# Performance work log

Measured on AMD Instinct MI355X. Metric: run time of the kernel, lower is better.

The kernel has to match this reference:

```python
import jax, jax.numpy as jnp
import numpy as np

N_HEAD = 12

def setup_inputs() -> dict:
    key = jax.random.key(0)
    k1, k2, k3, k4, k5 = jax.random.split(key, 5)
    B, T, C = 16, 1024, 768
    s = 0.02
    return {
        "x": jax.random.normal(k1, (B, T, C), dtype=jnp.float32),
        "W_attn": jax.random.normal(k2, (C, 3 * C), dtype=jnp.float32) * s,
        "b_attn": jax.random.normal(k3, (3 * C,), dtype=jnp.float32) * s,
        "W_proj": jax.random.normal(k4, (C, C), dtype=jnp.float32) * s,
        "b_proj": jax.random.normal(k5, (C,), dtype=jnp.float32) * s,
    }

def reference(x, W_attn, b_attn, W_proj, b_proj):
    B, T, C = x.shape
    H = N_HEAD
    d = C // H
    qkv = x @ W_attn + b_attn                      # [B,T,3C]
    q, k, v = jnp.split(qkv, 3, axis=-1)
    # [B,H,T,d]
    q = q.reshape(B, T, H, d).transpose(0, 2, 1, 3)
    k = k.reshape(B, T, H, d).transpose(0, 2, 1, 3)
    v = v.reshape(B, T, H, d).transpose(0, 2, 1, 3)
    scale = 1.0 / jnp.sqrt(jnp.array(d, dtype=x.dtype))
    att = jnp.einsum('bhqd,bhkd->bhqk', q, k) * scale   # [B,H,T,T]
    causal = jnp.tril(jnp.ones((T, T), dtype=bool))
    att = jnp.where(causal[None, None], att, -jnp.inf)
    att = jax.nn.softmax(att, axis=-1)
    # dropout is identity in eval mode (p=0 for deterministic reference)
    y = jnp.einsum('bhqk,bhkd->bhqd', att, v)            # [B,H,T,d]
    y = y.transpose(0, 2, 1, 3).reshape(B, T, C)
    return y @ W_proj + b_proj
```

## Files before the change

kernel.cpp:

```cpp
#include <hip/hip_runtime.h>
#include <cstddef>


typedef __bf16 bf16_t;
typedef __bf16 bf16x4 __attribute__((ext_vector_type(4)));
typedef __bf16 bf16x8 __attribute__((ext_vector_type(8)));
typedef float  f32x4  __attribute__((ext_vector_type(4)));

#define MFMA16(a,b,c) __builtin_amdgcn_mfma_f32_16x16x32_bf16((a),(b),(c),0,0,0)
#define GLOAD16(gp, lp) \
  __builtin_amdgcn_global_load_lds((const __attribute__((address_space(1))) unsigned int*)(gp), \
                                   (__attribute__((address_space(3))) unsigned int*)(lp), 16, 0, 0)

#define SWZ(row, c) (((row) * 64) + ((((c) ^ ((row) & 7)) * 8)))

#define QSCALE 0.1803368801111f

__global__ __launch_bounds__(256)
void prep_kernel(const float* __restrict__ x, bf16_t* __restrict__ Xb,
                 const float* __restrict__ Wa, bf16_t* __restrict__ WaT,
                 const float* __restrict__ Wp, bf16_t* __restrict__ WpT)
{
    __shared__ bf16_t tile[32][33];
    const int bx = blockIdx.x;
    if (bx < 12288) {
        const size_t i = ((size_t)bx * 256 + threadIdx.x) * 4;
        float4 f = *(const float4*)(x + i);
        bf16x4 o = {(bf16_t)f.x, (bf16_t)f.y, (bf16_t)f.z, (bf16_t)f.w};
        *(bf16x4*)(Xb + i) = o;
        return;
    }
    const float* in;  bf16_t* out;  int R, Cn, c0, r0;
    if (bx < 14016) {
        const int t = bx - 12288;
        in = Wa; out = WaT; R = 768; Cn = 2304;
        c0 = (t % 72) * 32; r0 = (t / 72) * 32;
    } else {
        const int t = bx - 14016;
        in = Wp; out = WpT; R = 768; Cn = 768;
        c0 = (t % 24) * 32; r0 = (t / 24) * 32;
    }
    const int tx = threadIdx.x & 31, ty = threadIdx.x >> 5;
#pragma unroll
    for (int i = 0; i < 4; ++i)
        tile[ty + i*8][tx] = (bf16_t)in[(size_t)(r0 + ty + i*8) * Cn + c0 + tx];
    __syncthreads();
#pragma unroll
    for (int i = 0; i < 4; ++i)
        out[(size_t)(c0 + ty + i*8) * R + r0 + tx] = tile[tx][ty + i*8];
}

#define LGKM0() asm volatile("s_waitcnt lgkmcnt(0)" ::: "memory")
#define VMC(n)  asm volatile("s_waitcnt vmcnt(" #n ")" ::: "memory")
#define PBAR()  __builtin_amdgcn_s_barrier()
#define PRIO1() __builtin_amdgcn_s_setprio(1)
#define PRIO0() __builtin_amdgcn_s_setprio(0)

#define STAGE_HT(buf, kt, ht) do { \
    if ((ht) == 0) { \
        const int r0_ = w * 16; \
        GLOAD16(WT + (size_t)(nt + r0_ + lr) * 768 + (kt) + lcs,     &Bs[buf][r0_ * 64]); \
        GLOAD16(WT + (size_t)(nt + r0_ + 8 + lr) * 768 + (kt) + lcs, &Bs[buf][(r0_ + 8) * 64]); \
    } else if ((ht) == 1) { \
        const int r1_ = 128 + w * 8; \
        GLOAD16(WT + (size_t)(nt + r1_ + lr) * 768 + (kt) + lcs,     &Bs[buf][r1_ * 64]); \
    } else { \
        const int r0_ = w * 16 + (((ht) == 3) ? 128 : 0); \
        GLOAD16(Xb + (size_t)(mt + r0_ + lr) * 768 + (kt) + lcs,     &As[buf][r0_ * 64]); \
        GLOAD16(Xb + (size_t)(mt + r0_ + 8 + lr) * 768 + (kt) + lcs, &As[buf][(r0_ + 8) * 64]); \
    } \
} while (0)

#define RD_BX(dst, buf) do { \
    _Pragma("unroll") for (int j_ = 0; j_ < 4; ++j_) \
    _Pragma("unroll") for (int ks_ = 0; ks_ < 2; ++ks_) \
        (dst)[j_][ks_] = *(const bf16x8*)(&As[buf][SWZ(wc * 64 + j_ * 16 + lm, ks_ * 4 + lq)]); \
} while (0)

#define RD_AW(dst, buf, F0, NF) do { \
    _Pragma("unroll") for (int p_ = 0; p_ < (NF); ++p_) \
    _Pragma("unroll") for (int ks_ = 0; ks_ < 2; ++ks_) \
        (dst)[p_][ks_] = *(const bf16x8*)(&Bs[buf][SWZ(wr * 96 + ((F0) + p_) * 16 + lm, ks_ * 4 + lq)]); \
} while (0)

#define MFMA_G(AW, BX, F0, NP) do { \
    _Pragma("unroll") for (int ks_ = 0; ks_ < 2; ++ks_) \
    _Pragma("unroll") for (int p_ = 0; p_ < (NP); ++p_) \
    _Pragma("unroll") for (int j_ = 0; j_ < 4; ++j_) \
        acc[(F0) + p_][j_] = MFMA16((AW)[p_][ks_], (BX)[j_][ks_], acc[(F0) + p_][j_]); \
} while (0)

__global__ __launch_bounds__(512)
void qkv_gemm8(const bf16_t* __restrict__ Xb, const bf16_t* __restrict__ WT,
               const float* __restrict__ bias,
               bf16_t* __restrict__ Qb, bf16_t* __restrict__ Kb, bf16_t* __restrict__ VT)
{
    __shared__ bf16_t As[2][256 * 64];
    __shared__ bf16_t Bs[2][192 * 64];
    const int tid = threadIdx.x;
    const int w = tid >> 6, l = tid & 63;
    const int lm = l & 15, lq = l >> 4;
    const int lr = l >> 3;
    const int lcs = ((l & 7) ^ lr) * 8;
    const int wr = w >> 2, wc = w & 3;

    const int g = blockIdx.x;
    const int gt = (g & 7) * 96 + (g >> 3);
    const int bm = gt / 12, bn = gt % 12;
    const int mt = bm * 256, nt = bn * 192;

    f32x4 acc[6][4];
    const f32x4 z4 = {0.f, 0.f, 0.f, 0.f};
#pragma unroll
    for (int i = 0; i < 6; ++i)
#pragma unroll
        for (int j = 0; j < 4; ++j) acc[i][j] = z4;

    bf16x8 bx0[4][2], bx1[4][2];
    bf16x8 aw01[2][2], aw23[2][2], aw45[2][2];

    STAGE_HT(0, 0, 0); STAGE_HT(0, 0, 1); STAGE_HT(0, 0, 2); STAGE_HT(0, 0, 3);
    STAGE_HT(1, 64, 0); STAGE_HT(1, 64, 1);
    VMC(3);
    PBAR();
    RD_BX(bx0, 0); RD_AW(aw01, 0, 0, 2);

#pragma unroll 1
    for (int it = 0; it < 5; ++it) {
        const int kv = it * 128 + 64, ku2 = kv + 64, kv2 = ku2 + 64;
        RD_AW(aw23, 0, 2, 2);
        STAGE_HT(1, kv, 2);
        PBAR(); LGKM0();
        PRIO1(); MFMA_G(aw01, bx0, 0, 2); PRIO0();
        PBAR();
        RD_AW(aw45, 0, 4, 2);
        STAGE_HT(1, kv, 3);
        PBAR(); LGKM0();
        PRIO1(); MFMA_G(aw23, bx0, 2, 2); PRIO0();
        PBAR();
        STAGE_HT(0, ku2, 0);
        PBAR();
        PRIO1(); MFMA_G(&aw45[0], bx0, 4, 1); PRIO0();
        VMC(2);
        PBAR();
        RD_BX(bx1, 1); RD_AW(aw01, 1, 0, 2);
        STAGE_HT(0, ku2, 1);
        PBAR(); LGKM0();
        PRIO1(); MFMA_G(&aw45[1], bx0, 5, 1); PRIO0();
        PBAR();
        RD_AW(aw23, 1, 2, 2);
        STAGE_HT(0, ku2, 2);
        PBAR(); LGKM0();
        PRIO1(); MFMA_G(aw01, bx1, 0, 2); PRIO0();
        PBAR();
        RD_AW(aw45, 1, 4, 2);
        STAGE_HT(0, ku2, 3);
        PBAR(); LGKM0();
        PRIO1(); MFMA_G(aw23, bx1, 2, 2); PRIO0();
        PBAR();
        STAGE_HT(1, kv2, 0);
        PBAR();
        PRIO1(); MFMA_G(&aw45[0], bx1, 4, 1); PRIO0();
        VMC(2);
        PBAR();
        RD_BX(bx0, 0); RD_AW(aw01, 0, 0, 2);
        STAGE_HT(1, kv2, 1);
        PBAR(); LGKM0();
        PRIO1(); MFMA_G(&aw45[1], bx1, 5, 1); PRIO0();
        PBAR();
    }

    RD_AW(aw23, 0, 2, 2);
    STAGE_HT(1, 704, 2);
    PBAR(); LGKM0();
    PRIO1(); MFMA_G(aw01, bx0, 0, 2); PRIO0();
    PBAR();
    RD_AW(aw45, 0, 4, 2);
    STAGE_HT(1, 704, 3);
    PBAR(); LGKM0();
    PRIO1(); MFMA_G(aw23, bx0, 2, 2); PRIO0();
    PBAR();
    PRIO1(); MFMA_G(&aw45[0], bx0, 4, 1); MFMA_G(&aw45[1], bx0, 5, 1); PRIO0();
    VMC(0);
    PBAR();
    RD_BX(bx1, 1); RD_AW(aw01, 1, 0, 2);
    RD_AW(aw23, 1, 2, 2); RD_AW(aw45, 1, 4, 2);
    LGKM0();
    MFMA_G(aw01, bx1, 0, 2);
    MFMA_G(aw23, bx1, 2, 2);
    MFMA_G(&aw45[0], bx1, 4, 1);
    MFMA_G(&aw45[1], bx1, 5, 1);

    const int which = nt / 768;
    const int b_ = mt >> 10;
    const int tb = (mt & 1023) + wc * 64;
    if (which == 2) {
#pragma unroll
        for (int f = 0; f < 6; ++f) {
            const int nglob = nt + wr * 96 + f * 16 + lq * 4;
            const int nin = nglob - 1536;
            const int h = nin >> 6, d0 = nin & 63;
            bf16_t* vt = VT + (size_t)(b_ * 12 + h) * 65536;
            const float4 bv = *(const float4*)(bias + nglob);
#pragma unroll
            for (int j = 0; j < 4; ++j) {
                const int t = tb + j * 16 + lm;
                f32x4 v = acc[f][j];
                vt[(size_t)(d0 + 0) * 1024 + t] = (bf16_t)(v[0] + bv.x);
                vt[(size_t)(d0 + 1) * 1024 + t] = (bf16_t)(v[1] + bv.y);
                vt[(size_t)(d0 + 2) * 1024 + t] = (bf16_t)(v[2] + bv.z);
                vt[(size_t)(d0 + 3) * 1024 + t] = (bf16_t)(v[3] + bv.w);
            }
        }
    } else {
        bf16_t* dst = (which == 0) ? Qb : Kb;
        const float qs = (which == 0) ? QSCALE : 1.0f;
#pragma unroll
        for (int f = 0; f < 6; ++f) {
            const int nglob = nt + wr * 96 + f * 16 + lq * 4;
            const int nin = nglob - which * 768;
            const int h = nin >> 6, d0 = nin & 63;
            const float4 bv = *(const float4*)(bias + nglob);
#pragma unroll
            for (int j = 0; j < 4; ++j) {
                const int t = tb + j * 16 + lm;
                f32x4 v = acc[f][j];
                bf16x4 o4 = {(bf16_t)((v[0] + bv.x) * qs), (bf16_t)((v[1] + bv.y) * qs),
                             (bf16_t)((v[2] + bv.z) * qs), (bf16_t)((v[3] + bv.w) * qs)};
                *(bf16x4*)(dst + ((size_t)(b_ * 12 + h) * 1024 + t) * 64 + d0) = o4;
            }
        }
    }
}

__global__ __launch_bounds__(256, 3)
void attn_kernel(const bf16_t* __restrict__ Qb, const bf16_t* __restrict__ Kb,
                 const bf16_t* __restrict__ VT, bf16_t* __restrict__ Y)
{
    __shared__ bf16_t Ks[2][64 * 64];
    __shared__ bf16_t Vs[2][64 * 64];
    __shared__ bf16_t Plds[4 * 16 * 72];
    const int tid = threadIdx.x;
    const int w = tid >> 6, l = tid & 63;
    const int lm = l & 15, lq = l >> 4;
    const int lr = l >> 3;
    const int lc8 = ((l & 7) ^ lr) * 8;
    const int xp = blockIdx.x;
    const int bh = blockIdx.y;
    const int loq = xp * 128, hiq = (7 - xp) * 128;

    int qmin[4];
    qmin[0] = loq + w * 32;      qmin[1] = qmin[0] + 16;
    qmin[2] = hiq + w * 32;      qmin[3] = qmin[2] + 16;

    const bf16_t* Kbase = Kb + (size_t)bh * 65536;
    const bf16_t* Vbase = VT + (size_t)bh * 65536;
    bf16_t* Pw = &Plds[w * 1152];
    const int r0a = w * 16, r0b = w * 16 + 8;

    bf16x8 bq[4][2];
#pragma unroll
    for (int m = 0; m < 4; ++m) {
        const bf16_t* Qp = Qb + ((size_t)bh * 1024 + qmin[m] + lm) * 64;
        bq[m][0] = *(const bf16x8*)(Qp + lq * 8);
        bq[m][1] = *(const bf16x8*)(Qp + 32 + lq * 8);
    }

    f32x4 O[4][4];
    float li[4] = {0.f, 0.f, 0.f, 0.f};
    const f32x4 z4 = {0.f, 0.f, 0.f, 0.f};
#pragma unroll
    for (int m = 0; m < 4; ++m)
#pragma unroll
        for (int s = 0; s < 4; ++s) O[m][s] = z4;

    const int kend = hiq + 64;

    GLOAD16(Kbase + (size_t)(r0a + lr) * 64 + lc8,   &Ks[0][r0a * 64]);
    GLOAD16(Kbase + (size_t)(r0b + lr) * 64 + lc8,   &Ks[0][r0b * 64]);
    GLOAD16(Vbase + (size_t)(r0a + lr) * 1024 + lc8, &Vs[0][r0a * 64]);
    GLOAD16(Vbase + (size_t)(r0b + lr) * 1024 + lc8, &Vs[0][r0b * 64]);
    __syncthreads();

    int cb = 0;
    for (int k0 = 0; k0 <= kend; k0 += 64) {
        const int nxt = cb ^ 1;
        if (k0 + 64 <= kend) {
            const int kn = k0 + 64;
            if (nxt) {
                GLOAD16(Kbase + (size_t)(kn + r0a + lr) * 64 + lc8,        &Ks[1][r0a * 64]);
                GLOAD16(Kbase + (size_t)(kn + r0b + lr) * 64 + lc8,        &Ks[1][r0b * 64]);
                GLOAD16(Vbase + (size_t)(r0a + lr) * 1024 + kn + lc8,      &Vs[1][r0a * 64]);
                GLOAD16(Vbase + (size_t)(r0b + lr) * 1024 + kn + lc8,      &Vs[1][r0b * 64]);
            } else {
                GLOAD16(Kbase + (size_t)(kn + r0a + lr) * 64 + lc8,        &Ks[0][r0a * 64]);
                GLOAD16(Kbase + (size_t)(kn + r0b + lr) * 64 + lc8,        &Ks[0][r0b * 64]);
                GLOAD16(Vbase + (size_t)(r0a + lr) * 1024 + kn + lc8,      &Vs[0][r0a * 64]);
                GLOAD16(Vbase + (size_t)(r0b + lr) * 1024 + kn + lc8,      &Vs[0][r0b * 64]);
            }
        }
        const bf16_t* Kc = Ks[cb];
        const bf16_t* Vc = Vs[cb];
#pragma unroll
        for (int m = 0; m < 4; ++m) {
            if (k0 > qmin[m] + 15) continue;
            f32x4 S[4];
#pragma unroll
            for (int s = 0; s < 4; ++s) S[s] = z4;
#pragma unroll
            for (int ks = 0; ks < 2; ++ks)
#pragma unroll
                for (int s = 0; s < 4; ++s) {
                    bf16x8 ak = *(const bf16x8*)(&Kc[SWZ(s * 16 + lm, ks * 4 + lq)]);
                    S[s] = MFMA16(ak, bq[m][ks], S[s]);
                }
            if (k0 + 63 > qmin[m]) {
                const int q = qmin[m] + lm;
#pragma unroll
                for (int s = 0; s < 4; ++s)
#pragma unroll
                    for (int rg = 0; rg < 4; ++rg)
                        if (k0 + s * 16 + lq * 4 + rg > q) S[s][rg] = -1e30f;
            }
            float ls = 0.f;
#pragma unroll
            for (int s = 0; s < 4; ++s)
#pragma unroll
                for (int rg = 0; rg < 4; ++rg) {
                    float pv = exp2f(S[s][rg]);
                    S[s][rg] = pv;
                    ls += pv;
                }
            li[m] += ls;
#pragma unroll
            for (int s = 0; s < 4; ++s) {
                bf16x4 p4 = {(bf16_t)S[s][0], (bf16_t)S[s][1],
                             (bf16_t)S[s][2], (bf16_t)S[s][3]};
                *(bf16x4*)(&Pw[lm * 72 + s * 16 + lq * 4]) = p4;
            }
#pragma unroll
            for (int ks = 0; ks < 2; ++ks) {
                bf16x8 bp = *(const bf16x8*)(&Pw[lm * 72 + ks * 32 + lq * 8]);
#pragma unroll
                for (int s = 0; s < 4; ++s) {
                    bf16x8 av = *(const bf16x8*)(&Vc[SWZ(s * 16 + lm, ks * 4 + lq)]);
                    O[m][s] = MFMA16(av, bp, O[m][s]);
                }
            }
        }
        __syncthreads();
        cb = nxt;
    }

    const int b = bh / 12, h = bh % 12;
#pragma unroll
    for (int m = 0; m < 4; ++m) {
        float s0 = li[m];
        s0 += __shfl_xor(s0, 16, 64);
        s0 += __shfl_xor(s0, 32, 64);
        const float inv = 1.f / s0;
        const size_t row = ((size_t)(b * 1024 + qmin[m] + lm)) * 768 + h * 64;
#pragma unroll
        for (int s = 0; s < 4; ++s) {
            bf16x4 y4 = {(bf16_t)(O[m][s][0] * inv), (bf16_t)(O[m][s][1] * inv),
                         (bf16_t)(O[m][s][2] * inv), (bf16_t)(O[m][s][3] * inv)};
            *(bf16x4*)(Y + row + s * 16 + lq * 4) = y4;
        }
    }
}

__global__ __launch_bounds__(256)
void proj_gemm(const bf16_t* __restrict__ A, const bf16_t* __restrict__ WT,
               const float* __restrict__ bias, float* __restrict__ out)
{
    __shared__ bf16_t As[128 * 64];
    __shared__ bf16_t Bs[128 * 64];
    const int tid = threadIdx.x;
    const int w = tid >> 6, l = tid & 63;
    const int lm = l & 15, lq = l >> 4;
    const int wy = w >> 1, wx = w & 1;
    const int lr = l >> 3;
    const int lcs = ((l & 7) ^ lr) * 8;
    const int nt = blockIdx.x * 128, mt = blockIdx.y * 128;

    f32x4 acc[4][4];
    const f32x4 z4 = {0.f, 0.f, 0.f, 0.f};
#pragma unroll
    for (int i = 0; i < 4; ++i)
#pragma unroll
        for (int j = 0; j < 4; ++j) acc[i][j] = z4;

    for (int kt = 0; kt < 768; kt += 64) {
#pragma unroll
        for (int p = 0; p < 4; ++p) {
            const int row = w * 32 + p * 8;
            GLOAD16(A  + (size_t)(mt + row + lr) * 768 + kt + lcs, &As[row * 64]);
            GLOAD16(WT + (size_t)(nt + row + lr) * 768 + kt + lcs, &Bs[row * 64]);
        }
        __syncthreads();
#pragma unroll
        for (int ks = 0; ks < 2; ++ks) {
            const int c = ks * 4 + lq;
            bf16x8 aw[4], bx[4];
#pragma unroll
            for (int i = 0; i < 4; ++i)
                aw[i] = *(const bf16x8*)(&Bs[SWZ(wx * 64 + i * 16 + lm, c)]);
#pragma unroll
            for (int j = 0; j < 4; ++j)
                bx[j] = *(const bf16x8*)(&As[SWZ(wy * 64 + j * 16 + lm, c)]);
#pragma unroll
            for (int i = 0; i < 4; ++i)
#pragma unroll
                for (int j = 0; j < 4; ++j)
                    acc[i][j] = MFMA16(aw[i], bx[j], acc[i][j]);
        }
        __syncthreads();
    }
#pragma unroll
    for (int i = 0; i < 4; ++i) {
        const int n0 = nt + wx * 64 + i * 16 + lq * 4;
        const float4 bv = *(const float4*)(bias + n0);
#pragma unroll
        for (int j = 0; j < 4; ++j) {
            const int t = mt + wy * 64 + j * 16 + lm;
            f32x4 v = acc[i][j];
            float4 o = {v[0] + bv.x, v[1] + bv.y, v[2] + bv.z, v[3] + bv.w};
            *(float4*)(out + (size_t)t * 768 + n0) = o;
        }
    }
}

extern "C" void kernel_launch(void* const* d_in, const int* in_sizes, int n_in,
                              void* d_out, int out_size, void* d_ws, size_t ws_size,
                              hipStream_t stream)
{
    const float* x      = (const float*)d_in[0];
    const float* W_attn = (const float*)d_in[1];
    const float* b_attn = (const float*)d_in[2];
    const float* W_proj = (const float*)d_in[3];
    const float* b_proj = (const float*)d_in[4];
    float* out = (float*)d_out;

    char* ws = (char*)d_ws;
    const size_t SZ = (size_t)16 * 12 * 1024 * 64 * 2;
    bf16_t* Qb  = (bf16_t*)(ws);
    bf16_t* Kb  = (bf16_t*)(ws + SZ);
    bf16_t* VT  = (bf16_t*)(ws + 3 * SZ);
    bf16_t* Yb  = (bf16_t*)(ws + 4 * SZ);
    bf16_t* Xb  = (bf16_t*)(ws + 4 * SZ);
    bf16_t* WaT = (bf16_t*)(ws + 5 * SZ);
    bf16_t* WpT = (bf16_t*)(ws + 5 * SZ + (size_t)2304 * 768 * 2);

    prep_kernel<<<14592, 256, 0, stream>>>(x, Xb, W_attn, WaT, W_proj, WpT);
    qkv_gemm8<<<768, 512, 0, stream>>>(Xb, WaT, b_attn, Qb, Kb, VT);
    attn_kernel<<<dim3(4, 192), 256, 0, stream>>>(Qb, Kb, VT, Yb);
    proj_gemm<<<dim3(6, 128), 256, 0, stream>>>(Yb, WpT, b_proj, out);
}
```

Baseline: 275.3 us.

## Reuse pipelined 256x192 GEMM for projection, swizzle attention P buffer

Moves the software-pipelined double-buffered GEMM body of the QKV kernel into a shared macro and uses it for a new 256x192-tile output projection kernel with grouped block ordering. This replaces the simple single-buffered 128x128 proj_gemm. The attention kernel's padded P scratch in LDS becomes an XOR-swizzled unpadded layout, and its occupancy hint rises from 3 to 4 blocks per CU. The projection now launches only 256 blocks, which may underfill the GPU, and the higher attention occupancy target may force register spills.

```diff
diff --git a/kernel.cpp b/kernel.cpp
--- a/kernel.cpp
+++ b/kernel.cpp
@@ -90,6 +90,77 @@
         acc[(F0) + p_][j_] = MFMA16((AW)[p_][ks_], (BX)[j_][ks_], acc[(F0) + p_][j_]); \
 } while (0)
 
+#define GEMM8_BODY() \
+    STAGE_HT(0, 0, 0); STAGE_HT(0, 0, 1); STAGE_HT(0, 0, 2); STAGE_HT(0, 0, 3); \
+    STAGE_HT(1, 64, 0); STAGE_HT(1, 64, 1); \
+    VMC(3); \
+    PBAR(); \
+    RD_BX(bx0, 0); RD_AW(aw01, 0, 0, 2); \
+    _Pragma("unroll 1") \
+    for (int it = 0; it < 5; ++it) { \
+        const int kv = it * 128 + 64, ku2 = kv + 64, kv2 = ku2 + 64; \
+        RD_AW(aw23, 0, 2, 2); \
+        STAGE_HT(1, kv, 2); \
+        PBAR(); LGKM0(); \
+        PRIO1(); MFMA_G(aw01, bx0, 0, 2); PRIO0(); \
+        PBAR(); \
+        RD_AW(aw45, 0, 4, 2); \
+        STAGE_HT(1, kv, 3); \
+        PBAR(); LGKM0(); \
+        PRIO1(); MFMA_G(aw23, bx0, 2, 2); PRIO0(); \
+        PBAR(); \
+        STAGE_HT(0, ku2, 0); \
+        PBAR(); \
+        PRIO1(); MFMA_G(&aw45[0], bx0, 4, 1); PRIO0(); \
+        VMC(2); \
+        PBAR(); \
+        RD_BX(bx1, 1); RD_AW(aw01, 1, 0, 2); \
+        STAGE_HT(0, ku2, 1); \
+        PBAR(); LGKM0(); \
+        PRIO1(); MFMA_G(&aw45[1], bx0, 5, 1); PRIO0(); \
+        PBAR(); \
+        RD_AW(aw23, 1, 2, 2); \
+        STAGE_HT(0, ku2, 2); \
+        PBAR(); LGKM0(); \
+        PRIO1(); MFMA_G(aw01, bx1, 0, 2); PRIO0(); \
+        PBAR(); \
+        RD_AW(aw45, 1, 4, 2); \
+        STAGE_HT(0, ku2, 3); \
+        PBAR(); LGKM0(); \
+        PRIO1(); MFMA_G(aw23, bx1, 2, 2); PRIO0(); \
+        PBAR(); \
+        STAGE_HT(1, kv2, 0); \
+        PBAR(); \
+        PRIO1(); MFMA_G(&aw45[0], bx1, 4, 1); PRIO0(); \
+        VMC(2); \
+        PBAR(); \
+        RD_BX(bx0, 0); RD_AW(aw01, 0, 0, 2); \
+        STAGE_HT(1, kv2, 1); \
+        PBAR(); LGKM0(); \
+        PRIO1(); MFMA_G(&aw45[1], bx1, 5, 1); PRIO0(); \
+        PBAR(); \
+    } \
+    RD_AW(aw23, 0, 2, 2); \
+    STAGE_HT(1, 704, 2); \
+    PBAR(); LGKM0(); \
+    PRIO1(); MFMA_G(aw01, bx0, 0, 2); PRIO0(); \
+    PBAR(); \
+    RD_AW(aw45, 0, 4, 2); \
+    STAGE_HT(1, 704, 3); \
+    PBAR(); LGKM0(); \
+    PRIO1(); MFMA_G(aw23, bx0, 2, 2); PRIO0(); \
+    PBAR(); \
+    PRIO1(); MFMA_G(&aw45[0], bx0, 4, 1); MFMA_G(&aw45[1], bx0, 5, 1); PRIO0(); \
+    VMC(0); \
+    PBAR(); \
+    RD_BX(bx1, 1); RD_AW(aw01, 1, 0, 2); \
+    RD_AW(aw23, 1, 2, 2); RD_AW(aw45, 1, 4, 2); \
+    LGKM0(); \
+    MFMA_G(aw01, bx1, 0, 2); \
+    MFMA_G(aw23, bx1, 2, 2); \
+    MFMA_G(&aw45[0], bx1, 4, 1); \
+    MFMA_G(&aw45[1], bx1, 5, 1);
+
 __global__ __launch_bounds__(512)
 void qkv_gemm8(const bf16_t* __restrict__ Xb, const bf16_t* __restrict__ WT,
                const float* __restrict__ bias,
@@ -119,77 +190,7 @@
     bf16x8 bx0[4][2], bx1[4][2];
     bf16x8 aw01[2][2], aw23[2][2], aw45[2][2];
 
-    STAGE_HT(0, 0, 0); STAGE_HT(0, 0, 1); STAGE_HT(0, 0, 2); STAGE_HT(0, 0, 3);
-    STAGE_HT(1, 64, 0); STAGE_HT(1, 64, 1);
-    VMC(3);
-    PBAR();
-    RD_BX(bx0, 0); RD_AW(aw01, 0, 0, 2);
-
-#pragma unroll 1
-    for (int it = 0; it < 5; ++it) {
-        const int kv = it * 128 + 64, ku2 = kv + 64, kv2 = ku2 + 64;
-        RD_AW(aw23, 0, 2, 2);
-        STAGE_HT(1, kv, 2);
-        PBAR(); LGKM0();
-        PRIO1(); MFMA_G(aw01, bx0, 0, 2); PRIO0();
-        PBAR();
-        RD_AW(aw45, 0, 4, 2);
-        STAGE_HT(1, kv, 3);
-        PBAR(); LGKM0();
-        PRIO1(); MFMA_G(aw23, bx0, 2, 2); PRIO0();
-        PBAR();
-        STAGE_HT(0, ku2, 0);
-        PBAR();
-        PRIO1(); MFMA_G(&aw45[0], bx0, 4, 1); PRIO0();
-        VMC(2);
-        PBAR();
-        RD_BX(bx1, 1); RD_AW(aw01, 1, 0, 2);
-        STAGE_HT(0, ku2, 1);
-        PBAR(); LGKM0();
-        PRIO1(); MFMA_G(&aw45[1], bx0, 5, 1); PRIO0();
-        PBAR();
-        RD_AW(aw23, 1, 2, 2);
-        STAGE_HT(0, ku2, 2);
-        PBAR(); LGKM0();
-        PRIO1(); MFMA_G(aw01, bx1, 0, 2); PRIO0();
-        PBAR();
-        RD_AW(aw45, 1, 4, 2);
-        STAGE_HT(0, ku2, 3);
-        PBAR(); LGKM0();
-        PRIO1(); MFMA_G(aw23, bx1, 2, 2); PRIO0();
-        PBAR();
-        STAGE_HT(1, kv2, 0);
-        PBAR();
-        PRIO1(); MFMA_G(&aw45[0], bx1, 4, 1); PRIO0();
-        VMC(2);
-        PBAR();
-        RD_BX(bx0, 0); RD_AW(aw01, 0, 0, 2);
-        STAGE_HT(1, kv2, 1);
-        PBAR(); LGKM0();
-        PRIO1(); MFMA_G(&aw45[1], bx1, 5, 1); PRIO0();
-        PBAR();
-    }
-
-    RD_AW(aw23, 0, 2, 2);
-    STAGE_HT(1, 704, 2);
-    PBAR(); LGKM0();
-    PRIO1(); MFMA_G(aw01, bx0, 0, 2); PRIO0();
-    PBAR();
-    RD_AW(aw45, 0, 4, 2);
-    STAGE_HT(1, 704, 3);
-    PBAR(); LGKM0();
-    PRIO1(); MFMA_G(aw23, bx0, 2, 2); PRIO0();
-    PBAR();
-    PRIO1(); MFMA_G(&aw45[0], bx0, 4, 1); MFMA_G(&aw45[1], bx0, 5, 1); PRIO0();
-    VMC(0);
-    PBAR();
-    RD_BX(bx1, 1); RD_AW(aw01, 1, 0, 2);
-    RD_AW(aw23, 1, 2, 2); RD_AW(aw45, 1, 4, 2);
-    LGKM0();
-    MFMA_G(aw01, bx1, 0, 2);
-    MFMA_G(aw23, bx1, 2, 2);
-    MFMA_G(&aw45[0], bx1, 4, 1);
-    MFMA_G(&aw45[1], bx1, 5, 1);
+    GEMM8_BODY();
 
     const int which = nt / 768;
     const int b_ = mt >> 10;
@@ -233,13 +234,58 @@
     }
 }
 
-__global__ __launch_bounds__(256, 3)
+__global__ __launch_bounds__(512)
+void proj_gemm8(const bf16_t* __restrict__ Xb, const bf16_t* __restrict__ WT,
+                const float* __restrict__ bias, float* __restrict__ out)
+{
+    __shared__ bf16_t As[2][256 * 64];
+    __shared__ bf16_t Bs[2][192 * 64];
+    const int tid = threadIdx.x;
+    const int w = tid >> 6, l = tid & 63;
+    const int lm = l & 15, lq = l >> 4;
+    const int lr = l >> 3;
+    const int lcs = ((l & 7) ^ lr) * 8;
+    const int wr = w >> 2, wc = w & 3;
+
+    const int g = blockIdx.x;
+    const int gt = (g & 7) * 32 + (g >> 3);
+    const int bm = gt >> 2, bn = gt & 3;
+    const int mt = bm * 256, nt = bn * 192;
+
+    f32x4 acc[6][4];
+    const f32x4 z4 = {0.f, 0.f, 0.f, 0.f};
+#pragma unroll
+    for (int i = 0; i < 6; ++i)
+#pragma unroll
+        for (int j = 0; j < 4; ++j) acc[i][j] = z4;
+
+    bf16x8 bx0[4][2], bx1[4][2];
+    bf16x8 aw01[2][2], aw23[2][2], aw45[2][2];
+
+    GEMM8_BODY();
+
+    const int tb = mt + wc * 64;
+#pragma unroll
+    for (int f = 0; f < 6; ++f) {
+        const int n0 = nt + wr * 96 + f * 16 + lq * 4;
+        const float4 bv = *(const float4*)(bias + n0);
+#pragma unroll
+        for (int j = 0; j < 4; ++j) {
+            const int t = tb + j * 16 + lm;
+            f32x4 v = acc[f][j];
+            float4 o = {v[0] + bv.x, v[1] + bv.y, v[2] + bv.z, v[3] + bv.w};
+            *(float4*)(out + (size_t)t * 768 + n0) = o;
+        }
+    }
+}
+
+__global__ __launch_bounds__(256, 4)
 void attn_kernel(const bf16_t* __restrict__ Qb, const bf16_t* __restrict__ Kb,
                  const bf16_t* __restrict__ VT, bf16_t* __restrict__ Y)
 {
     __shared__ bf16_t Ks[2][64 * 64];
     __shared__ bf16_t Vs[2][64 * 64];
-    __shared__ bf16_t Plds[4 * 16 * 72];
+    __shared__ bf16_t Plds[4 * 16 * 64];
     const int tid = threadIdx.x;
     const int w = tid >> 6, l = tid & 63;
     const int lm = l & 15, lq = l >> 4;
@@ -255,7 +301,7 @@
 
     const bf16_t* Kbase = Kb + (size_t)bh * 65536;
     const bf16_t* Vbase = VT + (size_t)bh * 65536;
-    bf16_t* Pw = &Plds[w * 1152];
+    bf16_t* Pw = &Plds[w * 1024];
     const int r0a = w * 16, r0b = w * 16 + 8;
 
     bf16x8 bq[4][2];
@@ -336,11 +382,11 @@
             for (int s = 0; s < 4; ++s) {
                 bf16x4 p4 = {(bf16_t)S[s][0], (bf16_t)S[s][1],
                              (bf16_t)S[s][2], (bf16_t)S[s][3]};
-                *(bf16x4*)(&Pw[lm * 72 + s * 16 + lq * 4]) = p4;
+                *(bf16x4*)(&Pw[SWZ(lm, 2 * s + (lq >> 1)) + (lq & 1) * 4]) = p4;
             }
 #pragma unroll
             for (int ks = 0; ks < 2; ++ks) {
-                bf16x8 bp = *(const bf16x8*)(&Pw[lm * 72 + ks * 32 + lq * 8]);
+                bf16x8 bp = *(const bf16x8*)(&Pw[SWZ(lm, 4 * ks + lq)]);
 #pragma unroll
                 for (int s = 0; s < 4; ++s) {
                     bf16x8 av = *(const bf16x8*)(&Vc[SWZ(s * 16 + lm, ks * 4 + lq)]);
@@ -365,67 +411,6 @@
             bf16x4 y4 = {(bf16_t)(O[m][s][0] * inv), (bf16_t)(O[m][s][1] * inv),
                          (bf16_t)(O[m][s][2] * inv), (bf16_t)(O[m][s][3] * inv)};
             *(bf16x4*)(Y + row + s * 16 + lq * 4) = y4;
-        }
-    }
-}
-
-__global__ __launch_bounds__(256)
-void proj_gemm(const bf16_t* __restrict__ A, const bf16_t* __restrict__ WT,
-               const float* __restrict__ bias, float* __restrict__ out)
-{
-    __shared__ bf16_t As[128 * 64];
-    __shared__ bf16_t Bs[128 * 64];
-    const int tid = threadIdx.x;
-    const int w = tid >> 6, l = tid & 63;
-    const int lm = l & 15, lq = l >> 4;
-    const int wy = w >> 1, wx = w & 1;
-    const int lr = l >> 3;
-    const int lcs = ((l & 7) ^ lr) * 8;
-    const int nt = blockIdx.x * 128, mt = blockIdx.y * 128;
-
-    f32x4 acc[4][4];
-    const f32x4 z4 = {0.f, 0.f, 0.f, 0.f};
-#pragma unroll
-    for (int i = 0; i < 4; ++i)
-#pragma unroll
-        for (int j = 0; j < 4; ++j) acc[i][j] = z4;
-
-    for (int kt = 0; kt < 768; kt += 64) {
-#pragma unroll
-        for (int p = 0; p < 4; ++p) {
-            const int row = w * 32 + p * 8;
-            GLOAD16(A  + (size_t)(mt + row + lr) * 768 + kt + lcs, &As[row * 64]);
-            GLOAD16(WT + (size_t)(nt + row + lr) * 768 + kt + lcs, &Bs[row * 64]);
-        }
-        __syncthreads();
-#pragma unroll
-        for (int ks = 0; ks < 2; ++ks) {
-            const int c = ks * 4 + lq;
-            bf16x8 aw[4], bx[4];
-#pragma unroll
-            for (int i = 0; i < 4; ++i)
-                aw[i] = *(const bf16x8*)(&Bs[SWZ(wx * 64 + i * 16 + lm, c)]);
-#pragma unroll
-            for (int j = 0; j < 4; ++j)
-                bx[j] = *(const bf16x8*)(&As[SWZ(wy * 64 + j * 16 + lm, c)]);
-#pragma unroll
-            for (int i = 0; i < 4; ++i)
-#pragma unroll
-                for (int j = 0; j < 4; ++j)
-                    acc[i][j] = MFMA16(aw[i], bx[j], acc[i][j]);
-        }
-        __syncthreads();
-    }
-#pragma unroll
-    for (int i = 0; i < 4; ++i) {
-        const int n0 = nt + wx * 64 + i * 16 + lq * 4;
-        const float4 bv = *(const float4*)(bias + n0);
-#pragma unroll
-        for (int j = 0; j < 4; ++j) {
-            const int t = mt + wy * 64 + j * 16 + lm;
-            f32x4 v = acc[i][j];
-            float4 o = {v[0] + bv.x, v[1] + bv.y, v[2] + bv.z, v[3] + bv.w};
-            *(float4*)(out + (size_t)t * 768 + n0) = o;
         }
     }
 }
@@ -454,5 +439,5 @@
     prep_kernel<<<14592, 256, 0, stream>>>(x, Xb, W_attn, WaT, W_proj, WpT);
     qkv_gemm8<<<768, 512, 0, stream>>>(Xb, WaT, b_attn, Qb, Kb, VT);
     attn_kernel<<<dim3(4, 192), 256, 0, stream>>>(Qb, Kb, VT, Yb);
-    proj_gemm<<<dim3(6, 128), 256, 0, stream>>>(Yb, WpT, b_proj, out);
+    proj_gemm8<<<256, 512, 0, stream>>>(Yb, WpT, b_proj, out);
 }
```

Result: slower. 359.5 us (+30.6%).
